# Optimization experiments

Hardware: AMD Instinct MI355X
Metric: run time of the kernel (lower is better)

## Reference

```python
import jax, jax.numpy as jnp
import numpy as np

N_NODES = 100000


def gcn_conv(x, W, b, src, dst, n):
    # PyG GCNConv: linear transform, add self-loops, symmetric deg^{-1/2} norm, scatter-sum.
    h = x @ W  # [N, out]
    loop = jnp.arange(n, dtype=src.dtype)
    s = jnp.concatenate([src, loop])
    d = jnp.concatenate([dst, loop])
    deg = jax.ops.segment_sum(jnp.ones_like(d, dtype=h.dtype), d, num_segments=n)
    dinv = jnp.where(deg > 0, jax.lax.rsqrt(deg), 0.0)
    norm = dinv[s] * dinv[d]  # [E+N]
    msg = h[s] * norm[:, None]  # gather + scale
    out = jax.ops.segment_sum(msg, d, num_segments=n)  # scatter-add
    return out + b


def setup_inputs() -> dict:
    key = jax.random.key(0)
    ks = jax.random.split(key, 6)
    in_dim, hid, out_dim = 128, 128, 32
    n_edges = 1600000
    x = jax.random.normal(ks[0], (N_NODES, in_dim), dtype=jnp.float32)
    edge_index = jax.random.randint(ks[1], (2, n_edges), 0, N_NODES, dtype=jnp.int64)
    W1 = jax.random.normal(ks[2], (in_dim, hid), dtype=jnp.float32) / np.sqrt(in_dim)
    b1 = jnp.zeros((hid,), dtype=jnp.float32)
    W2 = jax.random.normal(ks[3], (hid, out_dim), dtype=jnp.float32) / np.sqrt(hid)
    b2 = jnp.zeros((out_dim,), dtype=jnp.float32)
    return {"x": x, "edge_index": edge_index, "W1": W1, "b1": b1, "W2": W2, "b2": b2}


def reference(x, edge_index, W1, b1, W2, b2):
    src, dst = edge_index[0], edge_index[1]
    h = gcn_conv(x, W1, b1, src, dst, N_NODES)
    h = jax.nn.relu(h)
    # F.dropout(training=False) in eval -> identity
    h = gcn_conv(h, W2, b2, src, dst, N_NODES)
    return jax.nn.log_softmax(h, axis=1)
```

## Files before the change

### kernel.cpp

```cpp
#include <hip/hip_runtime.h>
#include <hip/hip_bf16.h>
#include <math.h>

#define N_NODES 100000
#define N_EDGES 1600000
#define NB 196
#define CAP 16000
#define CHUNK 4096

typedef unsigned int uint;
typedef unsigned short ushort_t;
typedef float f32x16 __attribute__((ext_vector_type(16)));
typedef float f32x2 __attribute__((ext_vector_type(2)));
typedef __bf16 bf16x8 __attribute__((ext_vector_type(8)));

__device__ __forceinline__ float bf2f(uint h) {
    union { uint u; float f; } x; x.u = h << 16; return x.f;
}
__device__ __forceinline__ unsigned short f2bf(float f) {
    union { float f; uint u; } x; x.f = f;
    uint u = x.u;
    return (unsigned short)((u + 0x7fffu + ((u >> 16) & 1u)) >> 16);
}
__device__ __forceinline__ uint pk2(float a, float b) {
    return (uint)f2bf(a) | ((uint)f2bf(b) << 16);
}
__device__ __forceinline__ bf16x8 bc8(uint4 u) { return __builtin_bit_cast(bf16x8, u); }

__device__ __forceinline__ int edge_at(const int* __restrict__ ei, int is32, long long idx) {
    return is32 ? ei[idx] : (int)(((const long long*)ei)[idx]);
}


__global__ __launch_bounds__(256) void k_bucket(const int* __restrict__ ei,
                                                const int* __restrict__ flag,
                                                int* __restrict__ cnt,
                                                uint* __restrict__ buf) {
    __shared__ uint stage[CHUNK];
    __shared__ unsigned char bid[CHUNK];
    __shared__ int lcnt[256], ls[256], lbase[256], gbase[256];
    int t = threadIdx.x;
    int is32 = *flag;
    lcnt[t] = 0;
    __syncthreads();
    int base = blockIdx.x * CHUNK;
    int srcv[16], dstv[16], offv[16];
    #pragma unroll
    for (int i = 0; i < 16; i++) {
        int e = base + i * 256 + t;
        if (e < N_EDGES) {
            srcv[i] = edge_at(ei, is32, e);
            dstv[i] = edge_at(ei, is32, (long long)N_EDGES + e);
            offv[i] = atomicAdd(&lcnt[dstv[i] >> 9], 1);
        } else {
            offv[i] = -1;
        }
    }
    __syncthreads();
    int c = lcnt[t];
    ls[t] = c;
    __syncthreads();
    int val = c;
    for (int off = 1; off < 256; off <<= 1) {
        int tmp = (t >= off) ? ls[t - off] : 0;
        __syncthreads();
        val += tmp;
        ls[t] = val;
        __syncthreads();
    }
    lbase[t] = val - c;
    if (c > 0) gbase[t] = atomicAdd(&cnt[t], c); else gbase[t] = 0;
    __syncthreads();
    int total = ls[255];
    #pragma unroll
    for (int i = 0; i < 16; i++) {
        if (offv[i] >= 0) {
            int b = dstv[i] >> 9;
            int p = lbase[b] + offv[i];
            stage[p] = (uint)srcv[i] | ((uint)(dstv[i] & 511) << 17);
            bid[p] = (unsigned char)b;
        }
    }
    __syncthreads();
    for (int idx = t; idx < total; idx += 256) {
        int b = bid[idx];
        int r = gbase[b] + (idx - lbase[b]);
        if (r < CAP) buf[(size_t)b * CAP + r] = stage[idx];
    }
}

__global__ void k_bscan(const int* __restrict__ cnt, int* __restrict__ bbase,
                        int* __restrict__ row_start) {
    __shared__ int s[256];
    int t = threadIdx.x;
    int v = (t < NB) ? cnt[t] : 0;
    s[t] = v;
    __syncthreads();
    int val = v;
    for (int off = 1; off < 256; off <<= 1) {
        int tmp = (t >= off) ? s[t - off] : 0;
        __syncthreads();
        val += tmp;
        s[t] = val;
        __syncthreads();
    }
    if (t < NB) bbase[t] = val - v;
    if (t == 0) row_start[N_NODES] = N_EDGES;
}

__global__ __launch_bounds__(256) void k_build(const uint* __restrict__ buf,
                                               const int* __restrict__ cnt,
                                               const int* __restrict__ bbase,
                                               int* __restrict__ row_start,
                                               float* __restrict__ dinv,
                                               int* __restrict__ csr_src) {
    __shared__ int ldeg[512], lexc[512], lcur[512], s[256];
    int t = threadIdx.x;
    int b = blockIdx.x;
    int n0 = b << 9;
    int nn = min(512, N_NODES - n0);
    int ne = min(cnt[b], CAP);
    const uint* __restrict__ in = buf + (size_t)b * CAP;
    int obase = bbase[b];
    ldeg[t] = 0; ldeg[t + 256] = 0;
    lcur[t] = 0; lcur[t + 256] = 0;
    __syncthreads();
    for (int idx = t; idx < ne; idx += 256) {
        atomicAdd(&ldeg[in[idx] >> 17], 1);
    }
    __syncthreads();
    int v = ldeg[2 * t] + ldeg[2 * t + 1];
    s[t] = v;
    __syncthreads();
    int val = v;
    for (int off = 1; off < 256; off <<= 1) {
        int tmp = (t >= off) ? s[t - off] : 0;
        __syncthreads();
        val += tmp;
        s[t] = val;
        __syncthreads();
    }
    int excl = val - v;
    lexc[2 * t] = excl;
    lexc[2 * t + 1] = excl + ldeg[2 * t];
    __syncthreads();
    for (int i = t; i < nn; i += 256) {
        row_start[n0 + i] = obase + lexc[i];
        dinv[n0 + i] = rsqrtf((float)(ldeg[i] + 1));
    }
    __syncthreads();
    for (int idx = t; idx < ne; idx += 256) {
        uint p = in[idx];
        int dl = p >> 17;
        int pos = obase + lexc[dl] + atomicAdd(&lcur[dl], 1);
        csr_src[pos] = (int)(p & 0x1FFFFu);
    }
}

__global__ void k_prep(const float* __restrict__ W1, const float* __restrict__ W2,
                       ushort_t* __restrict__ wt1, ushort_t* __restrict__ w2t,
                       const int* __restrict__ ei, int* __restrict__ flag) {
    int t = threadIdx.x;
    if (blockIdx.x == 0) {
        int v = ei[2 * t + 1] | ei[2 * (t + 256) + 1];
        if (v) atomicOr(flag, 1);
    }
    int i = blockIdx.x * 256 + t;
    if (i < 16384) {
        int c = i >> 7, k = i & 127;
        wt1[i] = f2bf(W1[k * 128 + c]);
    } else if (i < 20480) {
        int j = i - 16384;
        int c = j >> 7, p = j & 127;
        int cl = (p & 3) * 32 + (p >> 2);
        w2t[j] = f2bf(W2[cl * 32 + c]);
    }
}


__global__ __launch_bounds__(256) void k_gemm1(const float4* __restrict__ xf,
                                               const uint4* __restrict__ wt1,
                                               const float* __restrict__ dinv,
                                               uint* __restrict__ g1p) {
    __shared__ uint4 WT[128 * 16];
    int t = threadIdx.x;
    #pragma unroll
    for (int i = 0; i < 8; i++) {
        int gi = i * 256 + t;
        int c = gi >> 4, g = gi & 15;
        WT[c * 16 + (g ^ (c & 15))] = wt1[gi];
    }
    __syncthreads();
    int w = t >> 6, l = t & 63;
    int row0 = blockIdx.x * 128 + w * 32;
    int crow = min(row0 + (l & 31), N_NODES - 1);
    int hi = l >> 5;
    f32x16 acc[4];
    #pragma unroll
    for (int ct = 0; ct < 4; ct++)
        #pragma unroll
        for (int r = 0; r < 16; r++) acc[ct][r] = 0.0f;
    const float4* ap = xf + (size_t)crow * 32;
    #pragma unroll
    for (int k0 = 0; k0 < 8; k0++) {
        float4 f0 = ap[(k0 * 2 + hi) * 2];
        float4 f1 = ap[(k0 * 2 + hi) * 2 + 1];
        uint4 au;
        au.x = pk2(f0.x, f0.y); au.y = pk2(f0.z, f0.w);
        au.z = pk2(f1.x, f1.y); au.w = pk2(f1.z, f1.w);
        bf16x8 a = bc8(au);
        #pragma unroll
        for (int ct = 0; ct < 4; ct++) {
            int col = ct * 32 + (l & 31);
            bf16x8 b = bc8(WT[col * 16 + ((k0 * 2 + hi) ^ (col & 15))]);
            acc[ct] = __builtin_amdgcn_mfma_f32_32x32x16_bf16(a, b, acc[ct], 0, 0, 0);
        }
    }
    #pragma unroll
    for (int reg = 0; reg < 16; reg++) {
        int row = row0 + (reg & 3) + 8 * (reg >> 2) + 4 * hi;
        if (row < N_NODES) {
            float d = dinv[row];
            int pw = __builtin_amdgcn_cvt_pk_fp8_f32(acc[0][reg] * d, acc[1][reg] * d, 0, false);
            pw = __builtin_amdgcn_cvt_pk_fp8_f32(acc[2][reg] * d, acc[3][reg] * d, pw, true);
            g1p[(size_t)row * 32 + (l & 31)] = (uint)pw;
        }
    }
}

__global__ __launch_bounds__(256) void k_gemm2(const uint4* __restrict__ a1v,
                                               const uint4* __restrict__ w2t,
                                               const float* __restrict__ dinv,
                                               ushort_t* __restrict__ g2b) {
    __shared__ uint4 WT[32 * 16];
    int t = threadIdx.x;
    #pragma unroll
    for (int i = 0; i < 2; i++) {
        int gi = i * 256 + t;
        int c = gi >> 4, g = gi & 15;
        WT[c * 16 + (g ^ (c & 15))] = w2t[gi];
    }
    __syncthreads();
    int w = t >> 6, l = t & 63;
    int row0 = blockIdx.x * 128 + w * 32;
    int crow = min(row0 + (l & 31), N_NODES - 1);
    int hi = l >> 5;
    int col = l & 31;
    f32x16 acc;
    #pragma unroll
    for (int r = 0; r < 16; r++) acc[r] = 0.0f;
    const uint4* ap = a1v + (size_t)crow * 16;
    #pragma unroll
    for (int k0 = 0; k0 < 8; k0++) {
        bf16x8 a = bc8(ap[k0 * 2 + hi]);
        bf16x8 b = bc8(WT[col * 16 + ((k0 * 2 + hi) ^ (col & 15))]);
        acc = __builtin_amdgcn_mfma_f32_32x32x16_bf16(a, b, acc, 0, 0, 0);
    }
    #pragma unroll
    for (int reg = 0; reg < 16; reg++) {
        int row = row0 + (reg & 3) + 8 * (reg >> 2) + 4 * hi;
        if (row < N_NODES) g2b[(size_t)row * 32 + col] = f2bf(acc[reg] * dinv[row]);
    }
}


__global__ __launch_bounds__(256) void k_agg1(const uint2* __restrict__ g1p2,
                                              const float* __restrict__ dinv,
                                              const float* __restrict__ b1,
                                              const int* __restrict__ row_start,
                                              const int* __restrict__ csr_src,
                                              uint4* __restrict__ a1) {
    int v = blockIdx.x * 16 + (threadIdx.x >> 4);
    int L = threadIdx.x & 15;
    float s0, s1, s2, s3, s4, s5, s6, s7;
    {
        uint2 u = g1p2[(size_t)v * 16 + L];
        f32x2 a0 = __builtin_amdgcn_cvt_pk_f32_fp8(u.x, false);
        f32x2 a1f = __builtin_amdgcn_cvt_pk_f32_fp8(u.x, true);
        f32x2 a2 = __builtin_amdgcn_cvt_pk_f32_fp8(u.y, false);
        f32x2 a3 = __builtin_amdgcn_cvt_pk_f32_fp8(u.y, true);
        s0 = a0[0]; s1 = a0[1]; s2 = a1f[0]; s3 = a1f[1];
        s4 = a2[0]; s5 = a2[1]; s6 = a3[0]; s7 = a3[1];
    }
    int jb = row_start[v], je = row_start[v + 1];
    int j = jb;
    for (; j + 16 <= je; j += 16) {
        int idx[16];
        #pragma unroll
        for (int q = 0; q < 16; q++) idx[q] = csr_src[j + q];
        uint2 d[16];
        #pragma unroll
        for (int q = 0; q < 16; q++) d[q] = g1p2[(size_t)idx[q] * 16 + L];
        #pragma unroll
        for (int q = 0; q < 16; q++) {
            f32x2 a0 = __builtin_amdgcn_cvt_pk_f32_fp8(d[q].x, false);
            f32x2 a1f = __builtin_amdgcn_cvt_pk_f32_fp8(d[q].x, true);
            f32x2 a2 = __builtin_amdgcn_cvt_pk_f32_fp8(d[q].y, false);
            f32x2 a3 = __builtin_amdgcn_cvt_pk_f32_fp8(d[q].y, true);
            s0 += a0[0]; s1 += a0[1]; s2 += a1f[0]; s3 += a1f[1];
            s4 += a2[0]; s5 += a2[1]; s6 += a3[0]; s7 += a3[1];
        }
    }
    for (; j + 4 <= je; j += 4) {
        int idx[4];
        #pragma unroll
        for (int q = 0; q < 4; q++) idx[q] = csr_src[j + q];
        uint2 d[4];
        #pragma unroll
        for (int q = 0; q < 4; q++) d[q] = g1p2[(size_t)idx[q] * 16 + L];
        #pragma unroll
        for (int q = 0; q < 4; q++) {
            f32x2 a0 = __builtin_amdgcn_cvt_pk_f32_fp8(d[q].x, false);
            f32x2 a1f = __builtin_amdgcn_cvt_pk_f32_fp8(d[q].x, true);
            f32x2 a2 = __builtin_amdgcn_cvt_pk_f32_fp8(d[q].y, false);
            f32x2 a3 = __builtin_amdgcn_cvt_pk_f32_fp8(d[q].y, true);
            s0 += a0[0]; s1 += a0[1]; s2 += a1f[0]; s3 += a1f[1];
            s4 += a2[0]; s5 += a2[1]; s6 += a3[0]; s7 += a3[1];
        }
    }
    for (; j < je; j++) {
        uint2 u = g1p2[(size_t)csr_src[j] * 16 + L];
        f32x2 a0 = __builtin_amdgcn_cvt_pk_f32_fp8(u.x, false);
        f32x2 a1f = __builtin_amdgcn_cvt_pk_f32_fp8(u.x, true);
        f32x2 a2 = __builtin_amdgcn_cvt_pk_f32_fp8(u.y, false);
        f32x2 a3 = __builtin_amdgcn_cvt_pk_f32_fp8(u.y, true);
        s0 += a0[0]; s1 += a0[1]; s2 += a1f[0]; s3 += a1f[1];
        s4 += a2[0]; s5 += a2[1]; s6 += a3[0]; s7 += a3[1];
    }
    float d = dinv[v];
    int c0 = 2 * L;
    float o0 = fmaxf(d * s0 + b1[c0], 0.0f);
    float o1 = fmaxf(d * s1 + b1[32 + c0], 0.0f);
    float o2 = fmaxf(d * s2 + b1[64 + c0], 0.0f);
    float o3 = fmaxf(d * s3 + b1[96 + c0], 0.0f);
    float o4 = fmaxf(d * s4 + b1[c0 + 1], 0.0f);
    float o5 = fmaxf(d * s5 + b1[32 + c0 + 1], 0.0f);
    float o6 = fmaxf(d * s6 + b1[64 + c0 + 1], 0.0f);
    float o7 = fmaxf(d * s7 + b1[96 + c0 + 1], 0.0f);
    uint4 ow;
    ow.x = pk2(o0, o1); ow.y = pk2(o2, o3);
    ow.z = pk2(o4, o5); ow.w = pk2(o6, o7);
    a1[(size_t)v * 16 + L] = ow;
}

__global__ __launch_bounds__(256) void k_agg2(const uint* __restrict__ g2u,
                                              const float* __restrict__ dinv,
                                              const float* __restrict__ b2,
                                              const int* __restrict__ row_start,
                                              const int* __restrict__ csr_src,
                                              float2* __restrict__ out) {
    int v = blockIdx.x * 16 + (threadIdx.x >> 4);
    int L = threadIdx.x & 15;
    float acc0, acc1;
    {
        uint u = g2u[(size_t)v * 16 + L];
        acc0 = bf2f(u & 0xffffu); acc1 = bf2f(u >> 16);
    }
    int jb = row_start[v], je = row_start[v + 1];
    int j = jb;
    for (; j + 16 <= je; j += 16) {
        int idx[16];
        #pragma unroll
        for (int q = 0; q < 16; q++) idx[q] = csr_src[j + q];
        uint d[16];
        #pragma unroll
        for (int q = 0; q < 16; q++) d[q] = g2u[(size_t)idx[q] * 16 + L];
        #pragma unroll
        for (int q = 0; q < 16; q++) {
            acc0 += bf2f(d[q] & 0xffffu); acc1 += bf2f(d[q] >> 16);
        }
    }
    for (; j + 4 <= je; j += 4) {
        int idx[4];
        #pragma unroll
        for (int q = 0; q < 4; q++) idx[q] = csr_src[j + q];
        uint d[4];
        #pragma unroll
        for (int q = 0; q < 4; q++) d[q] = g2u[(size_t)idx[q] * 16 + L];
        #pragma unroll
        for (int q = 0; q < 4; q++) {
            acc0 += bf2f(d[q] & 0xffffu); acc1 += bf2f(d[q] >> 16);
        }
    }
    for (; j < je; j++) {
        uint u = g2u[(size_t)csr_src[j] * 16 + L];
        acc0 += bf2f(u & 0xffffu); acc1 += bf2f(u >> 16);
    }
    float dv = dinv[v];
    float z0 = dv * acc0 + b2[2 * L];
    float z1 = dv * acc1 + b2[2 * L + 1];
    float m = fmaxf(z0, z1);
    #pragma unroll
    for (int off = 8; off >= 1; off >>= 1) m = fmaxf(m, __shfl_xor(m, off));
    float e = __expf(z0 - m) + __expf(z1 - m);
    #pragma unroll
    for (int off = 8; off >= 1; off >>= 1) e += __shfl_xor(e, off);
    float lg = __logf(e);
    float2 o;
    o.x = (z0 - m) - lg;
    o.y = (z1 - m) - lg;
    out[(size_t)v * 16 + L] = o;
}


extern "C" void kernel_launch(void* const* d_in, const int* in_sizes, int n_in,
                              void* d_out, int out_size, void* d_ws, size_t ws_size,
                              hipStream_t stream) {
    const float* x  = (const float*)d_in[0];
    const int*   ei = (const int*)d_in[1];
    const float* W1 = (const float*)d_in[2];
    const float* b1 = (const float*)d_in[3];
    const float* W2 = (const float*)d_in[4];
    const float* b2 = (const float*)d_in[5];
    float* out = (float*)d_out;

    char* ws = (char*)d_ws;
    size_t off = 0;
    auto alloc = [&](size_t bytes) {
        void* p = ws + off;
        off = (off + bytes + 255) & ~255ULL;
        return p;
    };
    int* flag = (int*)alloc(4);
    int* cnt  = (int*)alloc((size_t)NB * 4);
    size_t zero_bytes = off;
    int*   bbase     = (int*)alloc((size_t)NB * 4);
    int*   row_start = (int*)alloc((size_t)(N_NODES + 1) * 4);
    float* dinv      = (float*)alloc((size_t)N_NODES * 4);
    int*   csr_src   = (int*)alloc((size_t)N_EDGES * 4);
    ushort_t* wt1g   = (ushort_t*)alloc(16384 * 2);
    ushort_t* w2tg   = (ushort_t*)alloc(4096 * 2);
    uint*  g1p       = (uint*)alloc((size_t)N_NODES * 128);
    size_t ubytes = (size_t)N_NODES * 128 * 2;
    void* uregion = alloc(ubytes);
    uint*  buf = (uint*)uregion;
    uint4* a1  = (uint4*)uregion;
    uint*  g2u = (uint*)g1p;

    hipMemsetAsync(flag, 0, zero_bytes, stream);

    k_prep<<<80, 256, 0, stream>>>(W1, W2, wt1g, w2tg, ei, flag);
    k_bucket<<<(N_EDGES + CHUNK - 1) / CHUNK, 256, 0, stream>>>(ei, flag, cnt, buf);
    k_bscan<<<1, 256, 0, stream>>>(cnt, bbase, row_start);
    k_build<<<NB, 256, 0, stream>>>(buf, cnt, bbase, row_start, dinv, csr_src);
    k_gemm1<<<(N_NODES + 127) / 128, 256, 0, stream>>>((const float4*)x, (const uint4*)wt1g, dinv, g1p);
    k_agg1<<<N_NODES / 16, 256, 0, stream>>>((const uint2*)g1p, dinv, b1, row_start, csr_src, a1);
    k_gemm2<<<(N_NODES + 127) / 128, 256, 0, stream>>>((const uint4*)a1, (const uint4*)w2tg, dinv, g2u ? (ushort_t*)g2u : nullptr);
    k_agg2<<<N_NODES / 16, 256, 0, stream>>>(g2u, dinv, b2, row_start, csr_src, (float2*)out);
}
```

Measured before the change: 157.2 us.

## Fuse second GEMM into layer-1 aggregation and store layer-2 features in fp8

Removes the separate bucket-scan and GEMM2 kernels: the scan is recomputed in every k_build block, and the 128x32 second linear layer runs in FP32 from LDS inside the agg1 epilogue. This avoids writing and re-reading the bf16 hidden activation. Layer-2 features are stored as fp8, and agg2 is reshaped to 8 lanes per node with float4 output, which cuts gather traffic. The cost is extra per-block W2 staging and scalar FMA work in agg1, plus extra quantization error from fp8.

```diff
diff --git a/kernel.cpp b/kernel.cpp
--- a/kernel.cpp
+++ b/kernel.cpp
@@ -89,39 +89,31 @@
     }
 }
 
-__global__ void k_bscan(const int* __restrict__ cnt, int* __restrict__ bbase,
-                        int* __restrict__ row_start) {
-    __shared__ int s[256];
-    int t = threadIdx.x;
-    int v = (t < NB) ? cnt[t] : 0;
-    s[t] = v;
-    __syncthreads();
-    int val = v;
-    for (int off = 1; off < 256; off <<= 1) {
-        int tmp = (t >= off) ? s[t - off] : 0;
-        __syncthreads();
-        val += tmp;
-        s[t] = val;
-        __syncthreads();
-    }
-    if (t < NB) bbase[t] = val - v;
-    if (t == 0) row_start[N_NODES] = N_EDGES;
-}
-
 __global__ __launch_bounds__(256) void k_build(const uint* __restrict__ buf,
                                                const int* __restrict__ cnt,
-                                               const int* __restrict__ bbase,
                                                int* __restrict__ row_start,
                                                float* __restrict__ dinv,
                                                int* __restrict__ csr_src) {
     __shared__ int ldeg[512], lexc[512], lcur[512], s[256];
     int t = threadIdx.x;
     int b = blockIdx.x;
+    int cv = (t < NB) ? cnt[t] : 0;
+    s[t] = cv;
+    __syncthreads();
+    int val = cv;
+    for (int off = 1; off < 256; off <<= 1) {
+        int tmp = (t >= off) ? s[t - off] : 0;
+        __syncthreads();
+        val += tmp;
+        s[t] = val;
+        __syncthreads();
+    }
+    int obase = (b == 0) ? 0 : s[b - 1];
+    if (b == 0 && t == 0) row_start[N_NODES] = N_EDGES;
     int n0 = b << 9;
     int nn = min(512, N_NODES - n0);
     int ne = min(cnt[b], CAP);
     const uint* __restrict__ in = buf + (size_t)b * CAP;
-    int obase = bbase[b];
     ldeg[t] = 0; ldeg[t + 256] = 0;
     lcur[t] = 0; lcur[t + 256] = 0;
     __syncthreads();
@@ -132,15 +124,15 @@
     int v = ldeg[2 * t] + ldeg[2 * t + 1];
     s[t] = v;
     __syncthreads();
-    int val = v;
+    int val2 = v;
     for (int off = 1; off < 256; off <<= 1) {
         int tmp = (t >= off) ? s[t - off] : 0;
         __syncthreads();
-        val += tmp;
-        s[t] = val;
-        __syncthreads();
-    }
-    int excl = val - v;
+        val2 += tmp;
+        s[t] = val2;
+        __syncthreads();
+    }
+    int excl = val2 - v;
     lexc[2 * t] = excl;
     lexc[2 * t + 1] = excl + ldeg[2 * t];
     __syncthreads();
@@ -157,8 +149,7 @@
     }
 }
 
-__global__ void k_prep(const float* __restrict__ W1, const float* __restrict__ W2,
-                       ushort_t* __restrict__ wt1, ushort_t* __restrict__ w2t,
+__global__ void k_prep(const float* __restrict__ W1, ushort_t* __restrict__ wt1,
                        const int* __restrict__ ei, int* __restrict__ flag) {
     int t = threadIdx.x;
     if (blockIdx.x == 0) {
@@ -166,17 +157,9 @@
         if (v) atomicOr(flag, 1);
     }
     int i = blockIdx.x * 256 + t;
-    if (i < 16384) {
-        int c = i >> 7, k = i & 127;
-        wt1[i] = f2bf(W1[k * 128 + c]);
-    } else if (i < 20480) {
-        int j = i - 16384;
-        int c = j >> 7, p = j & 127;
-        int cl = (p & 3) * 32 + (p >> 2);
-        w2t[j] = f2bf(W2[cl * 32 + c]);
-    }
-}
-
+    int c = i >> 7, k = i & 127;
+    wt1[i] = f2bf(W1[k * 128 + c]);
+}
 
 __global__ __launch_bounds__(256) void k_gemm1(const float4* __restrict__ xf,
                                                const uint4* __restrict__ wt1,
@@ -228,50 +211,21 @@
     }
 }
 
-__global__ __launch_bounds__(256) void k_gemm2(const uint4* __restrict__ a1v,
-                                               const uint4* __restrict__ w2t,
-                                               const float* __restrict__ dinv,
-                                               ushort_t* __restrict__ g2b) {
-    __shared__ uint4 WT[32 * 16];
-    int t = threadIdx.x;
-    #pragma unroll
-    for (int i = 0; i < 2; i++) {
-        int gi = i * 256 + t;
-        int c = gi >> 4, g = gi & 15;
-        WT[c * 16 + (g ^ (c & 15))] = w2t[gi];
-    }
-    __syncthreads();
-    int w = t >> 6, l = t & 63;
-    int row0 = blockIdx.x * 128 + w * 32;
-    int crow = min(row0 + (l & 31), N_NODES - 1);
-    int hi = l >> 5;
-    int col = l & 31;
-    f32x16 acc;
-    #pragma unroll
-    for (int r = 0; r < 16; r++) acc[r] = 0.0f;
-    const uint4* ap = a1v + (size_t)crow * 16;
-    #pragma unroll
-    for (int k0 = 0; k0 < 8; k0++) {
-        bf16x8 a = bc8(ap[k0 * 2 + hi]);
-        bf16x8 b = bc8(WT[col * 16 + ((k0 * 2 + hi) ^ (col & 15))]);
-        acc = __builtin_amdgcn_mfma_f32_32x32x16_bf16(a, b, acc, 0, 0, 0);
-    }
-    #pragma unroll
-    for (int reg = 0; reg < 16; reg++) {
-        int row = row0 + (reg & 3) + 8 * (reg >> 2) + 4 * hi;
-        if (row < N_NODES) g2b[(size_t)row * 32 + col] = f2bf(acc[reg] * dinv[row]);
-    }
-}
-
-
 __global__ __launch_bounds__(256) void k_agg1(const uint2* __restrict__ g1p2,
                                               const float* __restrict__ dinv,
                                               const float* __restrict__ b1,
+                                              const float* __restrict__ W2,
                                               const int* __restrict__ row_start,
                                               const int* __restrict__ csr_src,
-                                              uint4* __restrict__ a1) {
-    int v = blockIdx.x * 16 + (threadIdx.x >> 4);
-    int L = threadIdx.x & 15;
+                                              ushort_t* __restrict__ g2p) {
+    __shared__ float Ws2[128 * 32];
+    __shared__ float As[16][132];
+    int t = threadIdx.x;
+    #pragma unroll
+    for (int i = 0; i < 16; i++) Ws2[i * 256 + t] = W2[i * 256 + t];
+    int g = t >> 4;
+    int L = t & 15;
+    int v = blockIdx.x * 16 + g;
     float s0, s1, s2, s3, s4, s5, s6, s7;
     {
         uint2 u = g1p2[(size_t)v * 16 + L];
@@ -284,36 +238,27 @@
     }
     int jb = row_start[v], je = row_start[v + 1];
     int j = jb;
-    for (; j + 16 <= je; j += 16) {
-        int idx[16];
+    for (; j + 8 <= je; j += 8) {
+        int i0 = csr_src[j + 0], i1 = csr_src[j + 1];
+        int i2 = csr_src[j + 2], i3 = csr_src[j + 3];
+        int i4 = csr_src[j + 4], i5 = csr_src[j + 5];
+        int i6 = csr_src[j + 6], i7 = csr_src[j + 7];
+        uint2 d0 = g1p2[(size_t)i0 * 16 + L];
+        uint2 d1 = g1p2[(size_t)i1 * 16 + L];
+        uint2 d2 = g1p2[(size_t)i2 * 16 + L];
+        uint2 d3 = g1p2[(size_t)i3 * 16 + L];
+        uint2 d4 = g1p2[(size_t)i4 * 16 + L];
+        uint2 d5 = g1p2[(size_t)i5 * 16 + L];
+        uint2 d6 = g1p2[(size_t)i6 * 16 + L];
+        uint2 d7 = g1p2[(size_t)i7 * 16 + L];
         #pragma unroll
-        for (int q = 0; q < 16; q++) idx[q] = csr_src[j + q];
-        uint2 d[16];
-        #pragma unroll
-        for (int q = 0; q < 16; q++) d[q] = g1p2[(size_t)idx[q] * 16 + L];
-        #pragma unroll
-        for (int q = 0; q < 16; q++) {
-            f32x2 a0 = __builtin_amdgcn_cvt_pk_f32_fp8(d[q].x, false);
-            f32x2 a1f = __builtin_amdgcn_cvt_pk_f32_fp8(d[q].x, true);
-            f32x2 a2 = __builtin_amdgcn_cvt_pk_f32_fp8(d[q].y, false);
-            f32x2 a3 = __builtin_amdgcn_cvt_pk_f32_fp8(d[q].y, true);
-            s0 += a0[0]; s1 += a0[1]; s2 += a1f[0]; s3 += a1f[1];
-            s4 += a2[0]; s5 += a2[1]; s6 += a3[0]; s7 += a3[1];
-        }
-    }
-    for (; j + 4 <= je; j += 4) {
-        int idx[4];
-        #pragma unroll
-        for (int q = 0; q < 4; q++) idx[q] = csr_src[j + q];
-        uint2 d[4];
-        #pragma unroll
-        for (int q = 0; q < 4; q++) d[q] = g1p2[(size_t)idx[q] * 16 + L];
-        #pragma unroll
-        for (int q = 0; q < 4; q++) {
-            f32x2 a0 = __builtin_amdgcn_cvt_pk_f32_fp8(d[q].x, false);
-            f32x2 a1f = __builtin_amdgcn_cvt_pk_f32_fp8(d[q].x, true);
-            f32x2 a2 = __builtin_amdgcn_cvt_pk_f32_fp8(d[q].y, false);
-            f32x2 a3 = __builtin_amdgcn_cvt_pk_f32_fp8(d[q].y, true);
+        for (int q = 0; q < 8; q++) {
+            uint2 uu = q == 0 ? d0 : q == 1 ? d1 : q == 2 ? d2 : q == 3 ? d3
+                     : q == 4 ? d4 : q == 5 ? d5 : q == 6 ? d6 : d7;
+            f32x2 a0 = __builtin_amdgcn_cvt_pk_f32_fp8(uu.x, false);
+            f32x2 a1f = __builtin_amdgcn_cvt_pk_f32_fp8(uu.x, true);
+            f32x2 a2 = __builtin_amdgcn_cvt_pk_f32_fp8(uu.y, false);
+            f32x2 a3 = __builtin_amdgcn_cvt_pk_f32_fp8(uu.y, true);
             s0 += a0[0]; s1 += a0[1]; s2 += a1f[0]; s3 += a1f[1];
             s4 += a2[0]; s5 += a2[1]; s6 += a3[0]; s7 += a3[1];
         }
@@ -337,69 +282,90 @@
     float o5 = fmaxf(d * s5 + b1[32 + c0 + 1], 0.0f);
     float o6 = fmaxf(d * s6 + b1[64 + c0 + 1], 0.0f);
     float o7 = fmaxf(d * s7 + b1[96 + c0 + 1], 0.0f);
-    uint4 ow;
-    ow.x = pk2(o0, o1); ow.y = pk2(o2, o3);
-    ow.z = pk2(o4, o5); ow.w = pk2(o6, o7);
-    a1[(size_t)v * 16 + L] = ow;
-}
-
-__global__ __launch_bounds__(256) void k_agg2(const uint* __restrict__ g2u,
+    As[g][c0]          = o0;
+    As[g][32 + c0]     = o1;
+    As[g][64 + c0]     = o2;
+    As[g][96 + c0]     = o3;
+    As[g][c0 + 1]      = o4;
+    As[g][32 + c0 + 1] = o5;
+    As[g][64 + c0 + 1] = o6;
+    As[g][96 + c0 + 1] = o7;
+    __syncthreads();
+    float acc0 = 0.0f, acc1 = 0.0f;
+    #pragma unroll 8
+    for (int k = 0; k < 128; k++) {
+        float a = As[g][k];
+        acc0 += a * Ws2[k * 32 + c0];
+        acc1 += a * Ws2[k * 32 + c0 + 1];
+    }
+    int pw = __builtin_amdgcn_cvt_pk_fp8_f32(acc0 * d, acc1 * d, 0, false);
+    g2p[(size_t)v * 16 + L] = (ushort_t)(pw & 0xffff);
+}
+
+__global__ __launch_bounds__(256) void k_agg2(const uint* __restrict__ g2p4,
                                               const float* __restrict__ dinv,
                                               const float* __restrict__ b2,
                                               const int* __restrict__ row_start,
                                               const int* __restrict__ csr_src,
-                                              float2* __restrict__ out) {
-    int v = blockIdx.x * 16 + (threadIdx.x >> 4);
-    int L = threadIdx.x & 15;
-    float acc0, acc1;
+                                              float4* __restrict__ out) {
+    int v = blockIdx.x * 32 + (threadIdx.x >> 3);
+    int L = threadIdx.x & 7;
+    float s0, s1, s2, s3;
     {
-        uint u = g2u[(size_t)v * 16 + L];
-        acc0 = bf2f(u & 0xffffu); acc1 = bf2f(u >> 16);
+        uint u = g2p4[(size_t)v * 8 + L];
+        f32x2 a0 = __builtin_amdgcn_cvt_pk_f32_fp8(u, false);
+        f32x2 a1f = __builtin_amdgcn_cvt_pk_f32_fp8(u, true);
+        s0 = a0[0]; s1 = a0[1]; s2 = a1f[0]; s3 = a1f[1];
     }
     int jb = row_start[v], je = row_start[v + 1];
     int j = jb;
-    for (; j + 16 <= je; j += 16) {
-        int idx[16];
+    for (; j + 8 <= je; j += 8) {
+        int i0 = csr_src[j + 0], i1 = csr_src[j + 1];
+        int i2 = csr_src[j + 2], i3 = csr_src[j + 3];
+        int i4 = csr_src[j + 4], i5 = csr_src[j + 5];
+        int i6 = csr_src[j + 6], i7 = csr_src[j + 7];
+        uint d0 = g2p4[(size_t)i0 * 8 + L];
+        uint d1 = g2p4[(size_t)i1 * 8 + L];
+        uint d2 = g2p4[(size_t)i2 * 8 + L];
+        uint d3 = g2p4[(size_t)i3 * 8 + L];
+        uint d4 = g2p4[(size_t)i4 * 8 + L];
+        uint d5 = g2p4[(size_t)i5 * 8 + L];
+        uint d6 = g2p4[(size_t)i6 * 8 + L];
+        uint d7 = g2p4[(size_t)i7 * 8 + L];
         #pragma unroll
-        for (int q = 0; q < 16; q++) idx[q] = csr_src[j + q];
-        uint d[16];
-        #pragma unroll
-        for (int q = 0; q < 16; q++) d[q] = g2u[(size_t)idx[q] * 16 + L];
-        #pragma unroll
-        for (int q = 0; q < 16; q++) {
-            acc0 += bf2f(d[q] & 0xffffu); acc1 += bf2f(d[q] >> 16);
-        }
-    }
-    for (; j + 4 <= je; j += 4) {
-        int idx[4];
-        #pragma unroll
-        for (int q = 0; q < 4; q++) idx[q] = csr_src[j + q];
-        uint d[4];
-        #pragma unroll
-        for (int q = 0; q < 4; q++) d[q] = g2u[(size_t)idx[q] * 16 + L];
-        #pragma unroll
-        for (int q = 0; q < 4; q++) {
-            acc0 += bf2f(d[q] & 0xffffu); acc1 += bf2f(d[q] >> 16);
+        for (int q = 0; q < 8; q++) {
+            uint uu = q == 0 ? d0 : q == 1 ? d1 : q == 2 ? d2 : q == 3 ? d3
+                    : q == 4 ? d4 : q == 5 ? d5 : q == 6 ? d6 : d7;
+            f32x2 a0 = __builtin_amdgcn_cvt_pk_f32_fp8(uu, false);
+            f32x2 a1f = __builtin_amdgcn_cvt_pk_f32_fp8(uu, true);
+            s0 += a0[0]; s1 += a0[1]; s2 += a1f[0]; s3 += a1f[1];
         }
     }
     for (; j < je; j++) {
-        uint u = g2u[(size_t)csr_src[j] * 16 + L];
-        acc0 += bf2f(u & 0xffffu); acc1 += bf2f(u >> 16);
+        uint u = g2p4[(size_t)csr_src[j] * 8 + L];
+        f32x2 a0 = __builtin_amdgcn_cvt_pk_f32_fp8(u, false);
+        f32x2 a1f = __builtin_amdgcn_cvt_pk_f32_fp8(u, true);
+        s0 += a0[0]; s1 += a0[1]; s2 += a1f[0]; s3 += a1f[1];
     }
     float dv = dinv[v];
-    float z0 = dv * acc0 + b2[2 * L];
-    float z1 = dv * acc1 + b2[2 * L + 1];
-    float m = fmaxf(z0, z1);
-    #pragma unroll
-    for (int off = 8; off >= 1; off >>= 1) m = fmaxf(m, __shfl_xor(m, off));
-    float e = __expf(z0 - m) + __expf(z1 - m);
-    #pragma unroll
-    for (int off = 8; off >= 1; off >>= 1) e += __shfl_xor(e, off);
+    int c0 = 4 * L;
+    float z0 = dv * s0 + b2[c0];
+    float z1 = dv * s1 + b2[c0 + 1];
+    float z2 = dv * s2 + b2[c0 + 2];
+    float z3 = dv * s3 + b2[c0 + 3];
+    float m = fmaxf(fmaxf(z0, z1), fmaxf(z2, z3));
+    #pragma unroll
+    for (int off = 4; off >= 1; off >>= 1) m = fmaxf(m, __shfl_xor(m, off));
+    float e = __expf(z0 - m) + __expf(z1 - m) + __expf(z2 - m) + __expf(z3 - m);
+    #pragma unroll
+    for (int off = 4; off >= 1; off >>= 1) e += __shfl_xor(e, off);
     float lg = __logf(e);
-    float2 o;
+    float4 o;
     o.x = (z0 - m) - lg;
     o.y = (z1 - m) - lg;
-    out[(size_t)v * 16 + L] = o;
+    o.z = (z2 - m) - lg;
+    o.w = (z3 - m) - lg;
+    out[(size_t)v * 8 + L] = o;
 }
 
 
@@ -424,27 +390,20 @@
     int* flag = (int*)alloc(4);
     int* cnt  = (int*)alloc((size_t)NB * 4);
     size_t zero_bytes = off;
-    int*   bbase     = (int*)alloc((size_t)NB * 4);
     int*   row_start = (int*)alloc((size_t)(N_NODES + 1) * 4);
     float* dinv      = (float*)alloc((size_t)N_NODES * 4);
     int*   csr_src   = (int*)alloc((size_t)N_EDGES * 4);
     ushort_t* wt1g   = (ushort_t*)alloc(16384 * 2);
-    ushort_t* w2tg   = (ushort_t*)alloc(4096 * 2);
     uint*  g1p       = (uint*)alloc((size_t)N_NODES * 128);
-    size_t ubytes = (size_t)N_NODES * 128 * 2;
-    void* uregion = alloc(ubytes);
-    uint*  buf = (uint*)uregion;
-    uint4* a1  = (uint4*)uregion;
-    uint*  g2u = (uint*)g1p;
+    ushort_t* g2p    = (ushort_t*)alloc((size_t)N_NODES * 32);
+    uint*  buf       = (uint*)alloc((size_t)NB * CAP * 4);
 
     hipMemsetAsync(flag, 0, zero_bytes, stream);
 
-    k_prep<<<80, 256, 0, stream>>>(W1, W2, wt1g, w2tg, ei, flag);
+    k_prep<<<64, 256, 0, stream>>>(W1, wt1g, ei, flag);
     k_bucket<<<(N_EDGES + CHUNK - 1) / CHUNK, 256, 0, stream>>>(ei, flag, cnt, buf);
-    k_bscan<<<1, 256, 0, stream>>>(cnt, bbase, row_start);
-    k_build<<<NB, 256, 0, stream>>>(buf, cnt, bbase, row_start, dinv, csr_src);
+    k_build<<<NB, 256, 0, stream>>>(buf, cnt, row_start, dinv, csr_src);
     k_gemm1<<<(N_NODES + 127) / 128, 256, 0, stream>>>((const float4*)x, (const uint4*)wt1g, dinv, g1p);
-    k_agg1<<<N_NODES / 16, 256, 0, stream>>>((const uint2*)g1p, dinv, b1, row_start, csr_src, a1);
-    k_gemm2<<<(N_NODES + 127) / 128, 256, 0, stream>>>((const uint4*)a1, (const uint4*)w2tg, dinv, g2u ? (ushort_t*)g2u : nullptr);
-    k_agg2<<<N_NODES / 16, 256, 0, stream>>>(g2u, dinv, b2, row_start, csr_src, (float2*)out);
-}
+    k_agg1<<<N_NODES / 16, 256, 0, stream>>>((const uint2*)g1p, dinv, b1, W2, row_start, csr_src, g2p);
+    k_agg2<<<N_NODES / 32, 256, 0, stream>>>((const uint*)g2p, dinv, b2, row_start, csr_src, (float4*)out);
+}
```

New measurement: 156.5 us. About the same (-0.4%).

## Store layer-2 features as fp8 and fold block scan into build kernel

Applied to the files above, without the earlier changes.

The layer-2 transformed features are now stored as fp8 (one byte per channel) instead of bf16. This halves the bytes gathered per edge in the second aggregation, which is rewritten so 8 lanes each handle 4 channels of a node. The separate single-block bucket prefix-scan kernel is removed, and every build block now recomputes the scan of bucket counts itself, saving one launch. The costs are lower precision in the layer-2 messages and duplicated scan work in each of the 196 build blocks.

```diff
diff --git a/kernel.cpp b/kernel.cpp
--- a/kernel.cpp
+++ b/kernel.cpp
@@ -10,6 +10,7 @@
 
 typedef unsigned int uint;
 typedef unsigned short ushort_t;
+typedef unsigned char uchar_t;
 typedef float f32x16 __attribute__((ext_vector_type(16)));
 typedef float f32x2 __attribute__((ext_vector_type(2)));
 typedef __bf16 bf16x8 __attribute__((ext_vector_type(8)));
@@ -89,39 +90,31 @@
     }
 }
 
-__global__ void k_bscan(const int* __restrict__ cnt, int* __restrict__ bbase,
-                        int* __restrict__ row_start) {
-    __shared__ int s[256];
-    int t = threadIdx.x;
-    int v = (t < NB) ? cnt[t] : 0;
-    s[t] = v;
-    __syncthreads();
-    int val = v;
-    for (int off = 1; off < 256; off <<= 1) {
-        int tmp = (t >= off) ? s[t - off] : 0;
-        __syncthreads();
-        val += tmp;
-        s[t] = val;
-        __syncthreads();
-    }
-    if (t < NB) bbase[t] = val - v;
-    if (t == 0) row_start[N_NODES] = N_EDGES;
-}
-
 __global__ __launch_bounds__(256) void k_build(const uint* __restrict__ buf,
                                                const int* __restrict__ cnt,
-                                               const int* __restrict__ bbase,
                                                int* __restrict__ row_start,
                                                float* __restrict__ dinv,
                                                int* __restrict__ csr_src) {
     __shared__ int ldeg[512], lexc[512], lcur[512], s[256];
     int t = threadIdx.x;
     int b = blockIdx.x;
+    int cv = (t < NB) ? cnt[t] : 0;
+    s[t] = cv;
+    __syncthreads();
+    int val = cv;
+    for (int off = 1; off < 256; off <<= 1) {
+        int tmp = (t >= off) ? s[t - off] : 0;
+        __syncthreads();
+        val += tmp;
+        s[t] = val;
+        __syncthreads();
+    }
+    int obase = (b == 0) ? 0 : s[b - 1];
+    if (b == 0 && t == 0) row_start[N_NODES] = N_EDGES;
     int n0 = b << 9;
     int nn = min(512, N_NODES - n0);
     int ne = min(cnt[b], CAP);
     const uint* __restrict__ in = buf + (size_t)b * CAP;
-    int obase = bbase[b];
     ldeg[t] = 0; ldeg[t + 256] = 0;
     lcur[t] = 0; lcur[t + 256] = 0;
     __syncthreads();
@@ -132,15 +125,15 @@
     int v = ldeg[2 * t] + ldeg[2 * t + 1];
     s[t] = v;
     __syncthreads();
-    int val = v;
+    int val2 = v;
     for (int off = 1; off < 256; off <<= 1) {
         int tmp = (t >= off) ? s[t - off] : 0;
         __syncthreads();
-        val += tmp;
-        s[t] = val;
-        __syncthreads();
-    }
-    int excl = val - v;
+        val2 += tmp;
+        s[t] = val2;
+        __syncthreads();
+    }
+    int excl = val2 - v;
     lexc[2 * t] = excl;
     lexc[2 * t + 1] = excl + ldeg[2 * t];
     __syncthreads();
@@ -177,7 +170,6 @@
     }
 }
 
-
 __global__ __launch_bounds__(256) void k_gemm1(const float4* __restrict__ xf,
                                                const uint4* __restrict__ wt1,
                                                const float* __restrict__ dinv,
@@ -227,42 +219,6 @@
         }
     }
 }
-
-__global__ __launch_bounds__(256) void k_gemm2(const uint4* __restrict__ a1v,
-                                               const uint4* __restrict__ w2t,
-                                               const float* __restrict__ dinv,
-                                               ushort_t* __restrict__ g2b) {
-    __shared__ uint4 WT[32 * 16];
-    int t = threadIdx.x;
-    #pragma unroll
-    for (int i = 0; i < 2; i++) {
-        int gi = i * 256 + t;
-        int c = gi >> 4, g = gi & 15;
-        WT[c * 16 + (g ^ (c & 15))] = w2t[gi];
-    }
-    __syncthreads();
-    int w = t >> 6, l = t & 63;
-    int row0 = blockIdx.x * 128 + w * 32;
-    int crow = min(row0 + (l & 31), N_NODES - 1);
-    int hi = l >> 5;
-    int col = l & 31;
-    f32x16 acc;
-    #pragma unroll
-    for (int r = 0; r < 16; r++) acc[r] = 0.0f;
-    const uint4* ap = a1v + (size_t)crow * 16;
-    #pragma unroll
-    for (int k0 = 0; k0 < 8; k0++) {
-        bf16x8 a = bc8(ap[k0 * 2 + hi]);
-        bf16x8 b = bc8(WT[col * 16 + ((k0 * 2 + hi) ^ (col & 15))]);
-        acc = __builtin_amdgcn_mfma_f32_32x32x16_bf16(a, b, acc, 0, 0, 0);
-    }
-    #pragma unroll
-    for (int reg = 0; reg < 16; reg++) {
-        int row = row0 + (reg & 3) + 8 * (reg >> 2) + 4 * hi;
-        if (row < N_NODES) g2b[(size_t)row * 32 + col] = f2bf(acc[reg] * dinv[row]);
-    }
-}
-
 
 __global__ __launch_bounds__(256) void k_agg1(const uint2* __restrict__ g1p2,
                                               const float* __restrict__ dinv,
@@ -343,63 +299,109 @@
     a1[(size_t)v * 16 + L] = ow;
 }
 
-__global__ __launch_bounds__(256) void k_agg2(const uint* __restrict__ g2u,
+__global__ __launch_bounds__(256) void k_gemm2(const uint4* __restrict__ a1v,
+                                               const uint4* __restrict__ w2t,
+                                               const float* __restrict__ dinv,
+                                               uchar_t* __restrict__ g2p) {
+    __shared__ uint4 WT[32 * 16];
+    int t = threadIdx.x;
+    #pragma unroll
+    for (int i = 0; i < 2; i++) {
+        int gi = i * 256 + t;
+        int c = gi >> 4, g = gi & 15;
+        WT[c * 16 + (g ^ (c & 15))] = w2t[gi];
+    }
+    __syncthreads();
+    int w = t >> 6, l = t & 63;
+    int row0 = blockIdx.x * 128 + w * 32;
+    int crow = min(row0 + (l & 31), N_NODES - 1);
+    int hi = l >> 5;
+    int col = l & 31;
+    f32x16 acc;
+    #pragma unroll
+    for (int r = 0; r < 16; r++) acc[r] = 0.0f;
+    const uint4* ap = a1v + (size_t)crow * 16;
+    #pragma unroll
+    for (int k0 = 0; k0 < 8; k0++) {
+        bf16x8 a = bc8(ap[k0 * 2 + hi]);
+        bf16x8 b = bc8(WT[col * 16 + ((k0 * 2 + hi) ^ (col & 15))]);
+        acc = __builtin_amdgcn_mfma_f32_32x32x16_bf16(a, b, acc, 0, 0, 0);
+    }
+    #pragma unroll
+    for (int reg = 0; reg < 16; reg++) {
+        int row = row0 + (reg & 3) + 8 * (reg >> 2) + 4 * hi;
+        if (row < N_NODES) {
+            float z = acc[reg] * dinv[row];
+            int pw = __builtin_amdgcn_cvt_pk_fp8_f32(z, z, 0, false);
+            g2p[(size_t)row * 32 + col] = (uchar_t)(pw & 0xff);
+        }
+    }
+}
+
+__global__ __launch_bounds__(256) void k_agg2(const uint* __restrict__ g2p4,
                                               const float* __restrict__ dinv,
                                               const float* __restrict__ b2,
                                               const int* __restrict__ row_start,
                                               const int* __restrict__ csr_src,
-                                              float2* __restrict__ out) {
-    int v = blockIdx.x * 16 + (threadIdx.x >> 4);
-    int L = threadIdx.x & 15;
-    float acc0, acc1;
+                                              float4* __restrict__ out) {
+    int v = blockIdx.x * 32 + (threadIdx.x >> 3);
+    int L = threadIdx.x & 7;
+    float s0, s1, s2, s3;
     {
-        uint u = g2u[(size_t)v * 16 + L];
-        acc0 = bf2f(u & 0xffffu); acc1 = bf2f(u >> 16);
+        uint u = g2p4[(size_t)v * 8 + L];
+        f32x2 a0 = __builtin_amdgcn_cvt_pk_f32_fp8(u, false);
+        f32x2 a1f = __builtin_amdgcn_cvt_pk_f32_fp8(u, true);
+        s0 = a0[0]; s1 = a0[1]; s2 = a1f[0]; s3 = a1f[1];
     }
     int jb = row_start[v], je = row_start[v + 1];
     int j = jb;
-    for (; j + 16 <= je; j += 16) {
-        int idx[16];
-        #pragma unroll
-        for (int q = 0; q < 16; q++) idx[q] = csr_src[j + q];
-        uint d[16];
-        #pragma unroll
-        for (int q = 0; q < 16; q++) d[q] = g2u[(size_t)idx[q] * 16 + L];
-        #pragma unroll
-        for (int q = 0; q < 16; q++) {
-            acc0 += bf2f(d[q] & 0xffffu); acc1 += bf2f(d[q] >> 16);
-        }
-    }
-    for (; j + 4 <= je; j += 4) {
-        int idx[4];
-        #pragma unroll
-        for (int q = 0; q < 4; q++) idx[q] = csr_src[j + q];
-        uint d[4];
-        #pragma unroll
-        for (int q = 0; q < 4; q++) d[q] = g2u[(size_t)idx[q] * 16 + L];
-        #pragma unroll
-        for (int q = 0; q < 4; q++) {
-            acc0 += bf2f(d[q] & 0xffffu); acc1 += bf2f(d[q] >> 16);
+    for (; j + 8 <= je; j += 8) {
+        int i0 = csr_src[j + 0], i1 = csr_src[j + 1];
+        int i2 = csr_src[j + 2], i3 = csr_src[j + 3];
+        int i4 = csr_src[j + 4], i5 = csr_src[j + 5];
+        int i6 = csr_src[j + 6], i7 = csr_src[j + 7];
+        uint d0 = g2p4[(size_t)i0 * 8 + L];
+        uint d1 = g2p4[(size_t)i1 * 8 + L];
+        uint d2 = g2p4[(size_t)i2 * 8 + L];
+        uint d3 = g2p4[(size_t)i3 * 8 + L];
+        uint d4 = g2p4[(size_t)i4 * 8 + L];
+        uint d5 = g2p4[(size_t)i5 * 8 + L];
+        uint d6 = g2p4[(size_t)i6 * 8 + L];
+        uint d7 = g2p4[(size_t)i7 * 8 + L];
+        #pragma unroll
+        for (int q = 0; q < 8; q++) {
+            uint uu = q == 0 ? d0 : q == 1 ? d1 : q == 2 ? d2 : q == 3 ? d3
+                    : q == 4 ? d4 : q == 5 ? d5 : q == 6 ? d6 : d7;
+            f32x2 a0 = __builtin_amdgcn_cvt_pk_f32_fp8(uu, false);
+            f32x2 a1f = __builtin_amdgcn_cvt_pk_f32_fp8(uu, true);
+            s0 += a0[0]; s1 += a0[1]; s2 += a1f[0]; s3 += a1f[1];
         }
     }
     for (; j < je; j++) {
-        uint u = g2u[(size_t)csr_src[j] * 16 + L];
-        acc0 += bf2f(u & 0xffffu); acc1 += bf2f(u >> 16);
+        uint u = g2p4[(size_t)csr_src[j] * 8 + L];
+        f32x2 a0 = __builtin_amdgcn_cvt_pk_f32_fp8(u, false);
+        f32x2 a1f = __builtin_amdgcn_cvt_pk_f32_fp8(u, true);
+        s0 += a0[0]; s1 += a0[1]; s2 += a1f[0]; s3 += a1f[1];
     }
     float dv = dinv[v];
-    float z0 = dv * acc0 + b2[2 * L];
-    float z1 = dv * acc1 + b2[2 * L + 1];
-    float m = fmaxf(z0, z1);
-    #pragma unroll
-    for (int off = 8; off >= 1; off >>= 1) m = fmaxf(m, __shfl_xor(m, off));
-    float e = __expf(z0 - m) + __expf(z1 - m);
-    #pragma unroll
-    for (int off = 8; off >= 1; off >>= 1) e += __shfl_xor(e, off);
+    int c0 = 4 * L;
+    float z0 = dv * s0 + b2[c0];
+    float z1 = dv * s1 + b2[c0 + 1];
+    float z2 = dv * s2 + b2[c0 + 2];
+    float z3 = dv * s3 + b2[c0 + 3];
+    float m = fmaxf(fmaxf(z0, z1), fmaxf(z2, z3));
+    #pragma unroll
+    for (int off = 4; off >= 1; off >>= 1) m = fmaxf(m, __shfl_xor(m, off));
+    float e = __expf(z0 - m) + __expf(z1 - m) + __expf(z2 - m) + __expf(z3 - m);
+    #pragma unroll
+    for (int off = 4; off >= 1; off >>= 1) e += __shfl_xor(e, off);
     float lg = __logf(e);
-    float2 o;
+    float4 o;
     o.x = (z0 - m) - lg;
     o.y = (z1 - m) - lg;
-    out[(size_t)v * 16 + L] = o;
+    o.z = (z2 - m) - lg;
+    o.w = (z3 - m) - lg;
+    out[(size_t)v * 8 + L] = o;
 }
 
 
@@ -424,27 +426,24 @@
     int* flag = (int*)alloc(4);
     int* cnt  = (int*)alloc((size_t)NB * 4);
     size_t zero_bytes = off;
-    int*   bbase     = (int*)alloc((size_t)NB * 4);
     int*   row_start = (int*)alloc((size_t)(N_NODES + 1) * 4);
     float* dinv      = (float*)alloc((size_t)N_NODES * 4);
     int*   csr_src   = (int*)alloc((size_t)N_EDGES * 4);
     ushort_t* wt1g   = (ushort_t*)alloc(16384 * 2);
     ushort_t* w2tg   = (ushort_t*)alloc(4096 * 2);
     uint*  g1p       = (uint*)alloc((size_t)N_NODES * 128);
-    size_t ubytes = (size_t)N_NODES * 128 * 2;
-    void* uregion = alloc(ubytes);
+    void* uregion = alloc((size_t)N_NODES * 128 * 2);
     uint*  buf = (uint*)uregion;
     uint4* a1  = (uint4*)uregion;
-    uint*  g2u = (uint*)g1p;
+    uchar_t* g2p = (uchar_t*)g1p;
 
     hipMemsetAsync(flag, 0, zero_bytes, stream);
 
     k_prep<<<80, 256, 0, stream>>>(W1, W2, wt1g, w2tg, ei, flag);
     k_bucket<<<(N_EDGES + CHUNK - 1) / CHUNK, 256, 0, stream>>>(ei, flag, cnt, buf);
-    k_bscan<<<1, 256, 0, stream>>>(cnt, bbase, row_start);
-    k_build<<<NB, 256, 0, stream>>>(buf, cnt, bbase, row_start, dinv, csr_src);
+    k_build<<<NB, 256, 0, stream>>>(buf, cnt, row_start, dinv, csr_src);
     k_gemm1<<<(N_NODES + 127) / 128, 256, 0, stream>>>((const float4*)x, (const uint4*)wt1g, dinv, g1p);
     k_agg1<<<N_NODES / 16, 256, 0, stream>>>((const uint2*)g1p, dinv, b1, row_start, csr_src, a1);
-    k_gemm2<<<(N_NODES + 127) / 128, 256, 0, stream>>>((const uint4*)a1, (const uint4*)w2tg, dinv, g2u ? (ushort_t*)g2u : nullptr);
-    k_agg2<<<N_NODES / 16, 256, 0, stream>>>(g2u, dinv, b2, row_start, csr_src, (float2*)out);
-}
+    k_gemm2<<<(N_NODES + 127) / 128, 256, 0, stream>>>((const uint4*)a1, (const uint4*)w2tg, dinv, g2p);
+    k_agg2<<<N_NODES / 32, 256, 0, stream>>>((const uint*)g2p, dinv, b2, row_start, csr_src, (float4*)out);
+}
```

Result: faster. 147.1 us (-6.4%).
